# Kernel tuning notes

Measured on AMD Instinct MI355X. Metric: run time of the kernel, lower is better.

## Reference

```python
import jax, jax.numpy as jnp
import numpy as np

B, S, D, H, DFF = 2, 2048, 1024, 16, 4096
DK = D // H
EPS = 1e-6


def setup_inputs() -> dict:
    key = jax.random.key(0)
    ks = jax.random.split(key, 12)
    p = lambda k, shp: (jax.random.normal(k, shp, dtype=jnp.float32) * 0.02)
    return {
        "x": jax.random.normal(ks[0], (B, S, D), dtype=jnp.float32),
        "src_mask": jax.random.randint(ks[1], (B, 1, 1, S), 0, 2, dtype=jnp.int32),
        "wq": p(ks[2], (D, D)), "bq": jnp.zeros((D,), jnp.float32),
        "wk": p(ks[3], (D, D)), "bk": jnp.zeros((D,), jnp.float32),
        "wv": p(ks[4], (D, D)), "bv": jnp.zeros((D,), jnp.float32),
        "wo": p(ks[5], (D, D)), "bo": jnp.zeros((D,), jnp.float32),
        "w1": p(ks[6], (D, DFF)), "b1": jnp.zeros((DFF,), jnp.float32),
        "w2": p(ks[7], (DFF, D)), "b2": jnp.zeros((D,), jnp.float32),
        "a1": jnp.ones((1,), jnp.float32), "g1": jnp.zeros((1,), jnp.float32),
        "a2": jnp.ones((1,), jnp.float32), "g2": jnp.zeros((1,), jnp.float32),
    }


def _layernorm(x, alpha, bias):
    # Faithful to source: scalar alpha/bias, std with Bessel correction, eps on std
    mean = jnp.mean(x, axis=-1, keepdims=True)
    std = jnp.std(x, axis=-1, keepdims=True, ddof=1)
    return alpha * (x - mean) / (std + EPS) + bias


def _encoder_block(x, src_mask, wq, bq, wk, bk, wv, bv, wo, bo,
                   w1, b1, w2, b2, a1, g1, a2, g2):
    # --- self-attention sublayer (pre-norm residual) ---
    n = _layernorm(x, a1, g1)
    q = (n @ wq + bq).reshape(B, S, H, DK)
    k = (n @ wk + bk).reshape(B, S, H, DK)
    v = (n @ wv + bv).reshape(B, S, H, DK)
    scores = jnp.einsum("bqhd,bkhd->bhqk", q, k) / jnp.sqrt(jnp.float32(DK))
    scores = jnp.where(src_mask == 0, jnp.float32(-1e9), scores)
    attn = jax.nn.softmax(scores, axis=-1)
    ctx = jnp.einsum("bhqk,bkhd->bqhd", attn, v).reshape(B, S, D)
    x = x + (ctx @ wo + bo)
    # --- feed-forward sublayer (pre-norm residual) ---
    n2 = _layernorm(x, a2, g2)
    ff = jax.nn.relu(n2 @ w1 + b1) @ w2 + b2
    return x + ff


def reference(x, src_mask, wq, bq, wk, bk, wv, bv, wo, bo,
              w1, b1, w2, b2, a1, g1, a2, g2):
    return _encoder_block(x, src_mask, wq, bq, wk, bk, wv, bv, wo, bo,
                          w1, b1, w2, b2, a1, g1, a2, g2)
```

## Files before the change

kernel.cpp:

```cpp
#include <hip/hip_runtime.h>
#include <hip/hip_bf16.h>
#include <cstdint>

constexpr int Bc  = 2;
constexpr int Sc  = 2048;
constexpr int Dc  = 1024;
constexpr int Hc  = 16;
constexpr int DKc = 64;
constexpr int DFFc= 4096;
constexpr int BSc = Bc * Sc;

typedef __attribute__((ext_vector_type(8))) short bf16x8;
typedef __attribute__((ext_vector_type(4))) float f32x4;

__device__ __forceinline__ unsigned short f2bf(float x){
  union { float f; uint32_t u; } v; v.f = x;
  uint32_t r = v.u + 0x7fffu + ((v.u >> 16) & 1u);
  return (unsigned short)(r >> 16);
}

__device__ __forceinline__ void gload16(const void* g, void* l){
  __builtin_amdgcn_global_load_lds((const __attribute__((address_space(1))) void*)g,
                                   (__attribute__((address_space(3))) void*)l, 16, 0, 0);
}

__device__ __forceinline__ f32x4 mfma16(bf16x8 a, bf16x8 b, f32x4 c){
  return __builtin_amdgcn_mfma_f32_16x16x32_bf16(a, b, c, 0, 0, 0);
}

__device__ __forceinline__ uint32_t pk2bf(float lo, float hi){
  __hip_bfloat162 h = __float22bfloat162_rn(make_float2(lo, hi));
  return *reinterpret_cast<uint32_t*>(&h);
}

__device__ __forceinline__ float fexp2(float x){
  float r; asm("v_exp_f32 %0, %1" : "=v"(r) : "v"(x)); return r;
}

__device__ __forceinline__ int xcd_swz(int bid, int nwg){
  const int q = nwg >> 3, r = nwg & 7;
  const int xcd = bid & 7, idx = bid >> 3;
  return ((xcd < r) ? (xcd * (q + 1)) : (r * (q + 1) + (xcd - r) * q)) + idx;
}

__global__ __launch_bounds__(256)
void transpose_w(const float* __restrict__ in, unsigned short* __restrict__ out,
                 int K, int N){
  __shared__ float t[32][33];
  const int tx = threadIdx.x, ty = threadIdx.y;
  const int x0 = blockIdx.x * 32, y0 = blockIdx.y * 32;
#pragma unroll
  for (int j = ty; j < 32; j += 8) t[j][tx] = in[(long)(y0 + j) * N + x0 + tx];
  __syncthreads();
#pragma unroll
  for (int j = ty; j < 32; j += 8)
    out[(long)(x0 + j) * K + y0 + tx] = f2bf(t[tx][j]);
}

__global__ __launch_bounds__(256)
void concat_bias(const float* __restrict__ bq, const float* __restrict__ bk,
                 const float* __restrict__ bv, float* __restrict__ bqkv){
  int i = blockIdx.x * 256 + threadIdx.x;
  float v = (i < 1024) ? bq[i] : (i < 2048 ? bk[i - 1024] : bv[i - 2048]);
  bqkv[i] = v;
}

__global__ __launch_bounds__(256)
void mask_addend(const int* __restrict__ mask, float* __restrict__ madd){
  int i = blockIdx.x * 256 + threadIdx.x;
  madd[i] = (mask[i] != 0) ? 0.f : -1.442695e9f;
}

__global__ __launch_bounds__(256)
void layernorm_k(const float* __restrict__ x, const float* __restrict__ al,
                 const float* __restrict__ be, unsigned short* __restrict__ out){
  const int row = blockIdx.x, tid = threadIdx.x;
  const float4 v = ((const float4*)(x + (long)row * Dc))[tid];
  float s  = v.x + v.y + v.z + v.w;
  float ss = v.x*v.x + v.y*v.y + v.z*v.z + v.w*v.w;
#pragma unroll
  for (int d = 1; d < 64; d <<= 1){ s += __shfl_xor(s, d, 64); ss += __shfl_xor(ss, d, 64); }
  __shared__ float red[8];
  const int wid = tid >> 6, lane = tid & 63;
  if (lane == 0){ red[wid*2] = s; red[wid*2+1] = ss; }
  __syncthreads();
  s  = red[0] + red[2] + red[4] + red[6];
  ss = red[1] + red[3] + red[5] + red[7];
  const float mean = s * (1.f / 1024.f);
  float var = (ss - s * mean) * (1.f / 1023.f);
  var = fmaxf(var, 0.f);
  const float k = al[0] / (sqrtf(var) + 1e-6f);
  const float g = be[0];
  ushort4 o;
  o.x = f2bf((v.x - mean) * k + g);
  o.y = f2bf((v.y - mean) * k + g);
  o.z = f2bf((v.z - mean) * k + g);
  o.w = f2bf((v.w - mean) * k + g);
  ((ushort4*)(out + (long)row * Dc))[tid] = o;
}

template<int RELU, int OUTBF16, int RES>
__global__ __launch_bounds__(512, 2)
void gemm256(const unsigned short* __restrict__ A, const unsigned short* __restrict__ BT,
             const float* __restrict__ bias, const float* __restrict__ resid,
             void* __restrict__ Cout, int M, int N, int K){
  __shared__ unsigned short As[2][256 * 64];
  __shared__ unsigned short Bs[2][256 * 64];
  const int tid = threadIdx.x, wid = tid >> 6, lane = tid & 63;
  const int lg = lane >> 4, lr = lane & 15;
  const int wm = wid >> 2, wn = wid & 3;
  const int nwg = gridDim.x * gridDim.y;
  const int wg  = xcd_swz(blockIdx.y * gridDim.x + blockIdx.x, nwg);
  const int bx = wg % gridDim.x, by = wg / gridDim.x;
  const int m0 = by * 256, n0 = bx * 256;
  const long ldA = (long)K * 2;
  const f32x4 zero4 = {0.f, 0.f, 0.f, 0.f};
  f32x4 acc[8][4];
#pragma unroll
  for (int i = 0; i < 8; i++)
#pragma unroll
    for (int j = 0; j < 4; j++) acc[i][j] = zero4;

  const int obase0 = wid * 64 * 16;

  auto stage = [&](int b, int kt){
#pragma unroll
    for (int l = 0; l < 4; ++l){
      const int ob = l * 8192 + obase0;
      const int o  = ob + lane * 16;
      const int rr = o >> 7, c = (o >> 4) & 7;
      const long co = (long)kt * 128 + ((c ^ (rr & 7)) << 4);
      gload16((const char*)A  + (long)(m0 + rr) * ldA + co, (char*)As[b] + ob);
      gload16((const char*)BT + (long)(n0 + rr) * ldA + co, (char*)Bs[b] + ob);
    }
  };

  const int nt = K >> 6;
  stage(0, 0);
  stage(1, 1);

  int cur = 0;
  for (int t = 0; t < nt; ++t){
    if (t + 1 < nt) asm volatile("s_waitcnt vmcnt(8)" ::: "memory");
    else            asm volatile("s_waitcnt vmcnt(0)" ::: "memory");
    __builtin_amdgcn_s_barrier();
    __builtin_amdgcn_sched_barrier(0);
    const char* as = (const char*)As[cur];
    const char* bs = (const char*)Bs[cur];
    bf16x8 bfr[4][2];
#pragma unroll
    for (int ni = 0; ni < 4; ++ni){
      const int row = wn*64 + ni*16 + lr;
#pragma unroll
      for (int ks = 0; ks < 2; ++ks)
        bfr[ni][ks] = *reinterpret_cast<const bf16x8*>(bs + row*128 + (((ks*4 + lg) ^ (row & 7)) << 4));
    }
    __builtin_amdgcn_s_setprio(1);
#pragma unroll
    for (int mi = 0; mi < 8; ++mi){
      const int arow = wm*128 + mi*16 + lr;
      bf16x8 a0 = *reinterpret_cast<const bf16x8*>(as + arow*128 + (((0*4 + lg) ^ (arow & 7)) << 4));
      bf16x8 a1 = *reinterpret_cast<const bf16x8*>(as + arow*128 + (((1*4 + lg) ^ (arow & 7)) << 4));
#pragma unroll
      for (int ni = 0; ni < 4; ++ni){
        acc[mi][ni] = mfma16(a0, bfr[ni][0], acc[mi][ni]);
        acc[mi][ni] = mfma16(a1, bfr[ni][1], acc[mi][ni]);
      }
    }
    __builtin_amdgcn_s_setprio(0);
    __builtin_amdgcn_s_barrier();
    __builtin_amdgcn_sched_barrier(0);
    if (t + 2 < nt) stage(cur, t + 2);
    cur ^= 1;
  }

#pragma unroll
  for (int mi = 0; mi < 8; ++mi)
#pragma unroll
    for (int ni = 0; ni < 4; ++ni){
      const int col = n0 + wn*64 + ni*16 + lr;
      const float bc = bias[col];
#pragma unroll
      for (int r = 0; r < 4; ++r){
        const int row = m0 + wm*128 + mi*16 + lg*4 + r;
        float v = acc[mi][ni][r] + bc;
        if (RES)  v += resid[(long)row * N + col];
        if (RELU) v = fmaxf(v, 0.f);
        if (OUTBF16) ((unsigned short*)Cout)[(long)row * N + col] = f2bf(v);
        else         ((float*)Cout)[(long)row * N + col] = v;
      }
    }
}

template<int RELU, int OUTBF16, int RES, int PARTIAL>
__global__ __launch_bounds__(512, 2)
void gemm128(const unsigned short* __restrict__ A, const unsigned short* __restrict__ BT,
             const float* __restrict__ bias, const float* __restrict__ resid,
             void* __restrict__ Cout, float* __restrict__ p0,
             float* __restrict__ p1a, float* __restrict__ p1b,
             int M, int N, int K, int ldK){
  __shared__ unsigned short As[2][128 * 64];
  __shared__ unsigned short Bs[2][128 * 64];
  const int tid = threadIdx.x, wid = tid >> 6, lane = tid & 63;
  const int lg = lane >> 4, lr = lane & 15;
  const int wm = wid >> 2, wn = wid & 3;
  const int nwg = gridDim.x * gridDim.y;
  const int wg  = xcd_swz(blockIdx.y * gridDim.x + blockIdx.x, nwg);
  const int bx = wg % gridDim.x, by = wg / gridDim.x;
  const int m0 = by * 128, n0 = bx * 128;
  const int kc = PARTIAL ? blockIdx.z : 0;
  const unsigned short* Ab = A  + (long)kc * K;
  const unsigned short* Bb = BT + (long)kc * K;
  const long ldA = (long)ldK * 2;
  const f32x4 zero4 = {0.f, 0.f, 0.f, 0.f};
  f32x4 acc[4][2];
#pragma unroll
  for (int i = 0; i < 4; i++)
#pragma unroll
    for (int j = 0; j < 2; j++) acc[i][j] = zero4;

  auto stage = [&](int b, int kt){
#pragma unroll
    for (int l = 0; l < 2; ++l){
      const int ob = (wid*2 + l) * 1024;
      const int o  = ob + lane * 16;
      const int rr = o >> 7, c = (o >> 4) & 7;
      const long co = (long)kt * 128 + ((c ^ (rr & 7)) << 4);
      gload16((const char*)Ab + (long)(m0 + rr) * ldA + co, (char*)As[b] + ob);
      gload16((const char*)Bb + (long)(n0 + rr) * ldA + co, (char*)Bs[b] + ob);
    }
  };

  const int nt = K >> 6;
  stage(0, 0);
  stage(1, 1);

  int cur = 0;
  for (int t = 0; t < nt; ++t){
    if (t + 1 < nt) asm volatile("s_waitcnt vmcnt(4)" ::: "memory");
    else            asm volatile("s_waitcnt vmcnt(0)" ::: "memory");
    __builtin_amdgcn_s_barrier();
    __builtin_amdgcn_sched_barrier(0);
    const char* as = (const char*)As[cur];
    const char* bs = (const char*)Bs[cur];
    bf16x8 bfr[2][2];
#pragma unroll
    for (int ni = 0; ni < 2; ++ni){
      const int row = wn*32 + ni*16 + lr;
#pragma unroll
      for (int ks = 0; ks < 2; ++ks)
        bfr[ni][ks] = *reinterpret_cast<const bf16x8*>(bs + row*128 + (((ks*4 + lg) ^ (row & 7)) << 4));
    }
    __builtin_amdgcn_s_setprio(1);
#pragma unroll
    for (int mi = 0; mi < 4; ++mi){
      const int arow = wm*64 + mi*16 + lr;
      bf16x8 a0 = *reinterpret_cast<const bf16x8*>(as + arow*128 + (((0*4 + lg) ^ (arow & 7)) << 4));
      bf16x8 a1 = *reinterpret_cast<const bf16x8*>(as + arow*128 + (((1*4 + lg) ^ (arow & 7)) << 4));
#pragma unroll
      for (int ni = 0; ni < 2; ++ni){
        acc[mi][ni] = mfma16(a0, bfr[ni][0], acc[mi][ni]);
        acc[mi][ni] = mfma16(a1, bfr[ni][1], acc[mi][ni]);
      }
    }
    __builtin_amdgcn_s_setprio(0);
    __builtin_amdgcn_s_barrier();
    __builtin_amdgcn_sched_barrier(0);
    if (t + 2 < nt) stage(cur, t + 2);
    cur ^= 1;
  }

#pragma unroll
  for (int mi = 0; mi < 4; ++mi)
#pragma unroll
    for (int ni = 0; ni < 2; ++ni){
      const int col = n0 + wn*32 + ni*16 + lr;
      float bc = 0.f;
      if (!PARTIAL) bc = bias[col];
#pragma unroll
      for (int r = 0; r < 4; ++r){
        const int row = m0 + wm*64 + mi*16 + lg*4 + r;
        float v = acc[mi][ni][r] + bc;
        if (PARTIAL){
          float* pb = (kc == 0) ? p0 : ((row < 2048) ? p1a : (p1b - 2097152));
          pb[(long)row * N + col] = v;
        } else {
          if (RES)  v += resid[(long)row * N + col];
          if (RELU) v = fmaxf(v, 0.f);
          if (OUTBF16) ((unsigned short*)Cout)[(long)row * N + col] = f2bf(v);
          else         ((float*)Cout)[(long)row * N + col] = v;
        }
      }
    }
}

__global__ __launch_bounds__(256)
void reduce_ff2(const float* __restrict__ p0, const float* __restrict__ p1a,
                const float* __restrict__ p1b, const float* __restrict__ b2,
                float* __restrict__ out){
  const long n4 = (long)BSc * Dc / 4;
  for (long i = (long)blockIdx.x * 256 + threadIdx.x; i < n4; i += (long)gridDim.x * 256){
    const long flat = i * 4;
    const float4 a = ((const float4*)p0)[i];
    const float4 b = (flat < 2097152L) ? ((const float4*)p1a)[i]
                                       : ((const float4*)p1b)[i - 524288L];
    const float4 x = ((const float4*)out)[i];
    const float4 bb = ((const float4*)b2)[(flat & 1023) >> 2];
    float4 r;
    r.x = a.x + b.x + x.x + bb.x;
    r.y = a.y + b.y + x.y + bb.y;
    r.z = a.z + b.z + x.z + bb.z;
    r.w = a.w + b.w + x.w + bb.w;
    ((float4*)out)[i] = r;
  }
}

__global__ __launch_bounds__(256)
void transpose_v(const unsigned short* __restrict__ qkv, unsigned short* __restrict__ vt){
  __shared__ unsigned short tile[64][72];
  const int st = blockIdx.x * 64, bh = blockIdx.y;
  const int b = bh >> 4, h = bh & 15;
  const int tid = threadIdx.x;
  const int r = tid >> 2, c0 = (tid & 3) * 16;
  const unsigned short* src = qkv + ((long)(b*Sc + st + r) * 3072 + 2048 + h*64 + c0);
  *(uint4*)&tile[r][c0]     = *(const uint4*)src;
  *(uint4*)&tile[r][c0 + 8] = *(const uint4*)(src + 8);
  __syncthreads();
  union { unsigned short u[8]; uint4 v; } w0, w1;
#pragma unroll
  for (int j = 0; j < 8; j++){ w0.u[j] = tile[c0 + j][r]; w1.u[j] = tile[c0 + 8 + j][r]; }
  unsigned short* dst = vt + ((long)(bh*64 + r) * Sc + st + c0);
  *(uint4*)dst       = w0.v;
  *(uint4*)(dst + 8) = w1.v;
}

__global__ __launch_bounds__(512)
void attn_k(const unsigned short* __restrict__ qkv, const unsigned short* __restrict__ vt,
            const float* __restrict__ madd, unsigned short* __restrict__ ctx){
  __shared__ unsigned short Qs[128*64], Ks[2][64*64], Vs[2][64*64], Ps[8*16*64];
  const int tid = threadIdx.x, wid = tid >> 6, lane = tid & 63;
  const int lg = lane >> 4, lr = lane & 15;
  const int f   = blockIdx.y * gridDim.x + blockIdx.x;
  const int xcd = f & 7, j = f >> 3;
  const int bh  = (xcd << 2) | (j & 3);
  const int qt  = j >> 2;
  const int b = bh >> 4, h = bh & 15;
  const int s0 = qt * 128;
  const f32x4 zero4 = {0.f, 0.f, 0.f, 0.f};
  const short onebf = (short)0x3F80;
  const bf16x8 ones = {onebf, onebf, onebf, onebf, onebf, onebf, onebf, onebf};
  const float c1 = 0.18033688f;

  const char* kbase = (const char*)qkv + (long)(b*Sc) * 6144 + 2048 + h * 128;
  const char* vbase = (const char*)vt + (long)bh * 64 * 4096;
  const float* mrow = madd + b * Sc;
  unsigned short* pb = Ps + wid * 1024;

  auto stageKV = [&](int t, int bsel){
    const int o = wid * 1024;
    const int ol = o + lane * 16;
    const int r = ol >> 7, c = (ol >> 4) & 7;
    const int sw = ((c ^ (r & 7)) << 4);
    gload16(kbase + (long)(t*64 + r) * 6144 + sw, (char*)Ks[bsel] + o);
    gload16(vbase + (long)r * 4096 + t*128 + sw, (char*)Vs[bsel] + o);
  };

  const char* qbase = (const char*)qkv + ((long)(b*Sc + s0)) * 6144 + h * 128;
#pragma unroll
  for (int ld = 0; ld < 2; ++ld){
    const int o = (wid*2 + ld) * 1024;
    const int ol = o + lane * 16;
    const int r = ol >> 7, c = (ol >> 4) & 7;
    gload16(qbase + (long)r * 6144 + ((c ^ (r & 7)) << 4), (char*)Qs + o);
  }
  stageKV(0, 0);
  float4 ma[4];
#pragma unroll
  for (int ni = 0; ni < 4; ++ni) ma[ni] = *(const float4*)(mrow + ni*16 + lg*4);
  __syncthreads();
  bf16x8 qb[2];
#pragma unroll
  for (int ks = 0; ks < 2; ++ks){
    const int row = wid*16 + lr;
    qb[ks] = *reinterpret_cast<const bf16x8*>((const char*)Qs + row*128 + (((ks*4 + lg) ^ (row & 7)) << 4));
  }

  f32x4 acc[4] = {zero4, zero4, zero4, zero4};
  f32x4 accS = zero4;
  constexpr int NT = Sc / 64;

  for (int t = 0; t < NT; ++t){
    if (t){
      asm volatile("s_waitcnt vmcnt(0)" ::: "memory");
      __builtin_amdgcn_s_barrier();
      __builtin_amdgcn_sched_barrier(0);
    }
    if (t + 1 < NT) stageKV(t + 1, (t + 1) & 1);
    float4 man[4];
    if (t + 1 < NT){
#pragma unroll
      for (int ni = 0; ni < 4; ++ni) man[ni] = *(const float4*)(mrow + (t+1)*64 + ni*16 + lg*4);
    }

    const int cur = t & 1;
    const char* ksb = (const char*)Ks[cur];
    const char* vsb = (const char*)Vs[cur];

    f32x4 s4[4];
    __builtin_amdgcn_s_setprio(1);
#pragma unroll
    for (int ni = 0; ni < 4; ++ni){
      s4[ni] = zero4;
      const int row = ni*16 + lr;
#pragma unroll
      for (int ks = 0; ks < 2; ++ks){
        bf16x8 ak = *reinterpret_cast<const bf16x8*>(ksb + row*128 + (((ks*4 + lg) ^ (lr & 7)) << 4));
        s4[ni] = mfma16(ak, qb[ks], s4[ni]);
      }
    }
    __builtin_amdgcn_s_setprio(0);

    float p[4][4];
#pragma unroll
    for (int ni = 0; ni < 4; ++ni){
      p[ni][0] = fexp2(fmaf(s4[ni][0], c1, ma[ni].x));
      p[ni][1] = fexp2(fmaf(s4[ni][1], c1, ma[ni].y));
      p[ni][2] = fexp2(fmaf(s4[ni][2], c1, ma[ni].z));
      p[ni][3] = fexp2(fmaf(s4[ni][3], c1, ma[ni].w));
    }

#pragma unroll
    for (int ni = 0; ni < 4; ++ni){
      uint2 w;
      w.x = pk2bf(p[ni][0], p[ni][1]);
      w.y = pk2bf(p[ni][2], p[ni][3]);
      const int c = ni*2 + (lg >> 1);
      char* dst = (char*)pb + lr*128 + ((c ^ (lr & 7)) << 4) + (lg & 1) * 8;
      *(uint2*)dst = w;
    }
    bf16x8 pa[2];
#pragma unroll
    for (int ks = 0; ks < 2; ++ks){
      pa[ks] = *reinterpret_cast<const bf16x8*>((const char*)pb + lr*128 + (((ks*4 + lg) ^ (lr & 7)) << 4));
    }
    __builtin_amdgcn_s_setprio(1);
#pragma unroll
    for (int ks = 0; ks < 2; ++ks) accS = mfma16(pa[ks], ones, accS);
#pragma unroll
    for (int ni = 0; ni < 4; ++ni){
      const int row = ni*16 + lr;
#pragma unroll
      for (int ks = 0; ks < 2; ++ks){
        bf16x8 bv8 = *reinterpret_cast<const bf16x8*>(vsb + row*128 + (((ks*4 + lg) ^ (lr & 7)) << 4));
        acc[ni] = mfma16(pa[ks], bv8, acc[ni]);
      }
    }
    __builtin_amdgcn_s_setprio(0);
    if (t + 1 < NT){
#pragma unroll
      for (int ni = 0; ni < 4; ++ni) ma[ni] = man[ni];
    }
  }
#pragma unroll
  for (int ni = 0; ni < 4; ++ni){
    const int col = h*64 + ni*16 + lr;
#pragma unroll
    for (int r = 0; r < 4; ++r){
      const int row = s0 + wid*16 + lg*4 + r;
      ctx[(long)(b*Sc + row) * Dc + col] = f2bf(acc[ni][r] / accS[r]);
    }
  }
}

extern "C" void kernel_launch(void* const* d_in, const int* in_sizes, int n_in,
                              void* d_out, int out_size, void* d_ws, size_t ws_size,
                              hipStream_t stream){
  const float* x  = (const float*)d_in[0];
  const int* mask = (const int*)d_in[1];
  const float* wq = (const float*)d_in[2];
  const float* bq = (const float*)d_in[3];
  const float* wk = (const float*)d_in[4];
  const float* bk = (const float*)d_in[5];
  const float* wv = (const float*)d_in[6];
  const float* bv = (const float*)d_in[7];
  const float* wo = (const float*)d_in[8];
  const float* bo = (const float*)d_in[9];
  const float* w1 = (const float*)d_in[10];
  const float* b1 = (const float*)d_in[11];
  const float* w2 = (const float*)d_in[12];
  const float* b2 = (const float*)d_in[13];
  const float* a1 = (const float*)d_in[14];
  const float* g1 = (const float*)d_in[15];
  const float* a2 = (const float*)d_in[16];
  const float* g2 = (const float*)d_in[17];

  if (ws_size < 75509760u) return;

  char* ws = (char*)d_ws;
  unsigned short* wqkv_t = (unsigned short*)(ws + 0);
  unsigned short* wo_t   = (unsigned short*)(ws + 6291456);
  unsigned short* w1_t   = (unsigned short*)(ws + 8388608);
  unsigned short* w2_t   = (unsigned short*)(ws + 16777216);
  float*          bqkv   = (float*)(ws + 25165824);
  unsigned short* nbuf   = (unsigned short*)(ws + 25178112);
  float*          maddf  = (float*)(ws + 25178112);
  unsigned short* qkv    = (unsigned short*)(ws + 33566720);
  unsigned short* ff1    = (unsigned short*)(ws + 33566720);
  unsigned short* vt     = (unsigned short*)(ws + 58732544);
  unsigned short* ctx    = (unsigned short*)(ws + 67121152);
  float* p0  = (float*)(ws + 0);
  float* p1a = (float*)(ws + 25178112);
  float* p1b = (float*)(ws + 67121152);
  float* x2 = (float*)d_out;

  const dim3 tb(32, 8);
  transpose_w<<<dim3(32, 32),  tb, 0, stream>>>(wq, wqkv_t,            1024, 1024);
  transpose_w<<<dim3(32, 32),  tb, 0, stream>>>(wk, wqkv_t + 1048576,  1024, 1024);
  transpose_w<<<dim3(32, 32),  tb, 0, stream>>>(wv, wqkv_t + 2097152,  1024, 1024);
  transpose_w<<<dim3(32, 32),  tb, 0, stream>>>(wo, wo_t,              1024, 1024);
  transpose_w<<<dim3(128, 32), tb, 0, stream>>>(w1, w1_t,              1024, 4096);
  transpose_w<<<dim3(32, 128), tb, 0, stream>>>(w2, w2_t,              4096, 1024);
  concat_bias<<<12, 256, 0, stream>>>(bq, bk, bv, bqkv);

  layernorm_k<<<BSc, 256, 0, stream>>>(x, a1, g1, nbuf);
  gemm256<0,1,0><<<dim3(12, 16), 512, 0, stream>>>(nbuf, wqkv_t, bqkv, nullptr, qkv, BSc, 3072, 1024);
  mask_addend<<<16, 256, 0, stream>>>(mask, maddf);
  transpose_v<<<dim3(32, 32), 256, 0, stream>>>(qkv, vt);
  attn_k<<<dim3(16, 32), 512, 0, stream>>>(qkv, vt, maddf, ctx);
  gemm128<0,0,1,0><<<dim3(8, 32), 512, 0, stream>>>(ctx, wo_t, bo, x, x2,
                                                    nullptr, nullptr, nullptr, BSc, 1024, 1024, 1024);
  layernorm_k<<<BSc, 256, 0, stream>>>(x2, a2, g2, nbuf);
  gemm256<1,1,0><<<dim3(16, 16), 512, 0, stream>>>(nbuf, w1_t, b1, nullptr, ff1, BSc, 4096, 1024);
  gemm128<0,0,0,1><<<dim3(8, 32, 2), 512, 0, stream>>>(ff1, w2_t, nullptr, nullptr, nullptr,
                                                       p0, p1a, p1b, BSc, 1024, 2048, 4096);
  reduce_ff2<<<2048, 256, 0, stream>>>(p0, p1a, p1b, b2, (float*)d_out);
}
```

Baseline: 237.4 us.

## Interleave global-to-LDS prefetch of next K tile across four compute phases in GEMM

```diff
diff --git a/kernel.cpp b/kernel.cpp
--- a/kernel.cpp
+++ b/kernel.cpp
@@ -121,56 +121,72 @@
 #pragma unroll
     for (int j = 0; j < 4; j++) acc[i][j] = zero4;
 
-  const int obase0 = wid * 64 * 16;
-
-  auto stage = [&](int b, int kt){
-#pragma unroll
-    for (int l = 0; l < 4; ++l){
-      const int ob = l * 8192 + obase0;
+  auto stage_half = [&](int b, int kt, int h){
+    const unsigned short* src = (h < 2) ? A : BT;
+    const int rowg = ((h < 2) ? m0 : n0) + (h & 1) * 128;
+    char* dst = ((h < 2) ? (char*)As[b] : (char*)Bs[b]) + (h & 1) * 16384;
+#pragma unroll
+    for (int l = 0; l < 2; ++l){
+      const int ob = (wid*2 + l) * 1024;
       const int o  = ob + lane * 16;
       const int rr = o >> 7, c = (o >> 4) & 7;
       const long co = (long)kt * 128 + ((c ^ (rr & 7)) << 4);
-      gload16((const char*)A  + (long)(m0 + rr) * ldA + co, (char*)As[b] + ob);
-      gload16((const char*)BT + (long)(n0 + rr) * ldA + co, (char*)Bs[b] + ob);
+      gload16((const char*)src + (long)(rowg + rr) * ldA + co, dst + ob);
     }
   };
 
   const int nt = K >> 6;
-  stage(0, 0);
-  stage(1, 1);
+#pragma unroll
+  for (int h = 0; h < 4; ++h) stage_half(0, 0, h);
+  __syncthreads();
 
   int cur = 0;
   for (int t = 0; t < nt; ++t){
-    if (t + 1 < nt) asm volatile("s_waitcnt vmcnt(8)" ::: "memory");
-    else            asm volatile("s_waitcnt vmcnt(0)" ::: "memory");
-    __builtin_amdgcn_s_barrier();
-    __builtin_amdgcn_sched_barrier(0);
     const char* as = (const char*)As[cur];
     const char* bs = (const char*)Bs[cur];
     bf16x8 bfr[4][2];
 #pragma unroll
-    for (int ni = 0; ni < 4; ++ni){
-      const int row = wn*64 + ni*16 + lr;
-#pragma unroll
-      for (int ks = 0; ks < 2; ++ks)
-        bfr[ni][ks] = *reinterpret_cast<const bf16x8*>(bs + row*128 + (((ks*4 + lg) ^ (row & 7)) << 4));
-    }
-    __builtin_amdgcn_s_setprio(1);
-#pragma unroll
-    for (int mi = 0; mi < 8; ++mi){
-      const int arow = wm*128 + mi*16 + lr;
-      bf16x8 a0 = *reinterpret_cast<const bf16x8*>(as + arow*128 + (((0*4 + lg) ^ (arow & 7)) << 4));
-      bf16x8 a1 = *reinterpret_cast<const bf16x8*>(as + arow*128 + (((1*4 + lg) ^ (arow & 7)) << 4));
-#pragma unroll
-      for (int ni = 0; ni < 4; ++ni){
-        acc[mi][ni] = mfma16(a0, bfr[ni][0], acc[mi][ni]);
-        acc[mi][ni] = mfma16(a1, bfr[ni][1], acc[mi][ni]);
-      }
-    }
-    __builtin_amdgcn_s_setprio(0);
-    __builtin_amdgcn_s_barrier();
-    __builtin_amdgcn_sched_barrier(0);
-    if (t + 2 < nt) stage(cur, t + 2);
+    for (int p = 0; p < 4; ++p){
+      if (p == 0){
+#pragma unroll
+        for (int ni = 0; ni < 4; ++ni){
+          const int row = wn*64 + ni*16 + lr;
+#pragma unroll
+          for (int ks = 0; ks < 2; ++ks)
+            bfr[ni][ks] = *reinterpret_cast<const bf16x8*>(bs + row*128 + (((ks*4 + lg) ^ (row & 7)) << 4));
+        }
+      }
+      bf16x8 af[2][2];
+#pragma unroll
+      for (int i = 0; i < 2; ++i){
+        const int arow = wm*128 + (2*p + i)*16 + lr;
+        af[i][0] = *reinterpret_cast<const bf16x8*>(as + arow*128 + (((0*4 + lg) ^ (arow & 7)) << 4));
+        af[i][1] = *reinterpret_cast<const bf16x8*>(as + arow*128 + (((1*4 + lg) ^ (arow & 7)) << 4));
+      }
+      if (t + 1 < nt) stage_half(cur ^ 1, t + 1, p);
+      __builtin_amdgcn_sched_barrier(0);
+      __builtin_amdgcn_s_barrier();
+      asm volatile("s_waitcnt lgkmcnt(0)" ::: "memory");
+      __builtin_amdgcn_sched_barrier(0);
+      __builtin_amdgcn_s_setprio(1);
+#pragma unroll
+      for (int i = 0; i < 2; ++i){
+        const int mi = 2*p + i;
+#pragma unroll
+        for (int ni = 0; ni < 4; ++ni){
+          acc[mi][ni] = mfma16(af[i][0], bfr[ni][0], acc[mi][ni]);
+          acc[mi][ni] = mfma16(af[i][1], bfr[ni][1], acc[mi][ni]);
+        }
+      }
+      __builtin_amdgcn_s_setprio(0);
+      __builtin_amdgcn_sched_barrier(0);
+      __builtin_amdgcn_s_barrier();
+    }
+    if (t + 1 < nt){
+      asm volatile("s_waitcnt vmcnt(0)" ::: "memory");
+      __builtin_amdgcn_s_barrier();
+      __builtin_amdgcn_sched_barrier(0);
+    }
     cur ^= 1;
   }
 
```

Measured after the change: 237.2 us. About the same (-0.1%).
